# Kernel optimization log

Hardware: AMD Instinct MI355X
Metric: run time of the kernel (lower is better)

Reference implementation:

```python
import jax, jax.numpy as jnp
import numpy as np

B, N, NP, NS = 4, 8192, 2048, 32
CIN, COUT = 128, 256
RADIUS = 0.2
RELU_ALPHA = 0.2
BN_EPS = 1e-5


def setup_inputs() -> dict:
    key = jax.random.key(0)
    k1, k2, k3, k4, k5, k6, k7 = jax.random.split(key, 7)
    xyz = jax.random.uniform(k1, (B, N, 3), dtype=jnp.float32)          # points in unit cube
    feats = jax.random.normal(k2, (B, CIN, N), dtype=jnp.float32)
    conv_w = jax.random.normal(k3, (COUT, CIN), dtype=jnp.float32) * 0.05  # 1x1 conv kernel (bias off: bn=True)
    gamma = jax.random.uniform(k4, (COUT,), minval=0.5, maxval=1.5)
    beta = jax.random.normal(k5, (COUT,)) * 0.1
    rmean = jax.random.normal(k6, (COUT,)) * 0.1                        # BN running mean (eval mode)
    rvar = jax.random.uniform(k7, (COUT,), minval=0.5, maxval=1.5)      # BN running var
    return dict(xyz=xyz, feats=feats, conv_w=conv_w, gamma=gamma,
                beta=beta, rmean=rmean, rvar=rvar)


def _fps(pts):
    """Furthest point sampling. pts: [N,3] -> [NP] int32 indices. Starts at index 0 (CUDA kernel convention)."""
    mind0 = jnp.sum((pts - pts[0]) ** 2, axis=-1)  # [N]

    def step(mind, _):
        i = jnp.argmax(mind)
        mind = jnp.minimum(mind, jnp.sum((pts - pts[i]) ** 2, axis=-1))
        return mind, i.astype(jnp.int32)

    _, idxs = jax.lax.scan(step, mind0, None, length=NP - 1)
    return jnp.concatenate([jnp.zeros((1,), jnp.int32), idxs])


def reference(xyz, feats, conv_w, gamma, beta, rmean, rvar):
    # --- furthest point sampling + gather centroids ---
    fidx = jax.vmap(_fps)(xyz)                                   # [B,NP]
    new_xyz = jnp.take_along_axis(xyz, fidx[:, :, None], axis=1)  # [B,NP,3]

    # --- ball query: first NS point indices (in order) with dist^2 < r^2, pad with first hit ---
    d2 = jnp.sum((new_xyz[:, :, None, :] - xyz[:, None, :, :]) ** 2, axis=-1)  # [B,NP,N]
    mask = d2 < (RADIUS * RADIUS)
    key_ = jnp.where(mask, jnp.arange(N, dtype=jnp.float32), jnp.float32(N))
    neg, _ = jax.lax.top_k(-key_, NS)                            # NS smallest keys
    idx = (-neg).astype(jnp.int32)                               # [B,NP,NS], ascending index order
    first = idx[..., :1]
    fallback = jnp.where(first < N, first, 0)                    # empty ball -> index 0 (kernel default)
    idx = jnp.where(idx < N, idx, fallback)

    # --- grouping + max pool over neighbors ---
    gped = jax.vmap(lambda f, i: f[:, i])(feats, idx)            # [B,CIN,NP,NS]
    pooled = jnp.max(gped, axis=-1)                              # [B,CIN,NP]

    # --- 1x1 conv (no bias) + BatchNorm (eval) + LeakyReLU ---
    out = jnp.einsum('oc,bcn->bon', conv_w, pooled)              # [B,COUT,NP]
    inv = gamma / jnp.sqrt(rvar + BN_EPS)
    out = out * inv[None, :, None] + (beta - rmean * inv)[None, :, None]
    return jax.nn.leaky_relu(out, RELU_ALPHA)
```

## Files before the change

### kernel.cpp

```cpp
#include <hip/hip_runtime.h>
#include <cstdint>
#include <cstddef>

#define BB 4
#define NN 8192
#define NPP 2048
#define NSS 32
#define CINN 128
#define COUTT 256

template<int CTRL>
static __device__ __forceinline__ int dppi(int v){
  return __builtin_amdgcn_update_dpp(0, v, CTRL, 0xF, 0xF, true);
}
template<int CTRL>
static __device__ __forceinline__ float dppf(float v){
  return __int_as_float(__builtin_amdgcn_update_dpp(0, __float_as_int(v), CTRL, 0xF, 0xF, true));
}
static __device__ __forceinline__ float wave_max63(float v){
  v = fmaxf(v, dppf<0xB1>(v));
  v = fmaxf(v, dppf<0x4E>(v));
  v = fmaxf(v, dppf<0x141>(v));
  v = fmaxf(v, dppf<0x140>(v));
  v = fmaxf(v, dppf<0x142>(v));
  v = fmaxf(v, dppf<0x143>(v));
  return v;
}
static __device__ __forceinline__ int wave_mini63(int v){
  v = min(v, dppi<0xB1>(v));
  v = min(v, dppi<0x4E>(v));
  v = min(v, dppi<0x141>(v));
  v = min(v, dppi<0x140>(v));
  v = min(v, dppi<0x142>(v));
  v = min(v, dppi<0x143>(v));
  return v;
}
static __device__ __forceinline__ float red8_maxf(float v){
  v = fmaxf(v, dppf<0xB1>(v));
  v = fmaxf(v, dppf<0x4E>(v));
  v = fmaxf(v, dppf<0x141>(v));
  return v;
}
static __device__ __forceinline__ int red8_mini(int v){
  v = min(v, dppi<0xB1>(v));
  v = min(v, dppi<0x4E>(v));
  v = min(v, dppi<0x141>(v));
  return v;
}

__global__ __launch_bounds__(512)
void k_pre(const float* __restrict__ xyz, const float* __restrict__ feats,
           const float* __restrict__ convw,
           int* __restrict__ fidx, float* __restrict__ featsT, float* __restrict__ wT)
{
  __shared__ float smem[3*NN + 64];
  const int tid = threadIdx.x;
  const int blk = blockIdx.x;

  if (blk < BB) {
    const int b = blk;
    float* xs = smem;
    float* ys = smem + NN;
    float* zs = smem + 2*NN;
    float2* slots = (float2*)(smem + 3*NN);

    for (int n = tid; n < NN; n += 512){
      const float* p = xyz + ((size_t)b*NN + n)*3;
      xs[n] = p[0]; ys[n] = p[1]; zs[n] = p[2];
    }
    __syncthreads();

    float px[16], py[16], pz[16], mind[16];
    const int base = tid*16;
    #pragma unroll
    for (int j=0;j<16;++j){
      px[j]=xs[base+j]; py[j]=ys[base+j]; pz[j]=zs[base+j];
      mind[j]=3.0e38f;
    }
    int cur = 0;
    if (tid == 0) fidx[b*NPP] = 0;
    const int lane = tid & 63;
    const int wid  = tid >> 6;

    for (int s = 1; s < NPP; ++s){
      const float cx = xs[cur], cy = ys[cur], cz = zs[cur];
      float bv = -1.0f; int bj = 0;
      #pragma unroll
      for (int j=0;j<16;++j){
        const float dx = px[j]-cx, dy = py[j]-cy, dz = pz[j]-cz;
        const float d2 = fmaf(dz,dz, fmaf(dy,dy, dx*dx));
        const float m  = fminf(mind[j], d2);
        mind[j] = m;
        const bool g = m > bv;
        bv = g ? m : bv;
        bj = g ? j : bj;
      }
      const int bi = base + bj;

      float wm = wave_max63(bv);
      wm = __int_as_float(__builtin_amdgcn_readlane(__float_as_int(wm), 63));
      int cand = (bv == wm) ? bi : 0x7FFFFFFF;
      int wi = wave_mini63(cand);
      wi = __builtin_amdgcn_readlane(wi, 63);

      const int par = s & 1;
      if (lane == 0) slots[par*8 + wid] = make_float2(wm, __int_as_float(wi));
      __syncthreads();

      const float2 sv = slots[par*8 + (lane & 7)];
      const float v8 = sv.x;
      const int   i8 = __float_as_int(sv.y);
      const float gm = red8_maxf(v8);
      const int   c8 = (v8 == gm) ? i8 : 0x7FFFFFFF;
      cur = red8_mini(c8);

      if (tid == 0) fidx[b*NPP + s] = cur;
    }
  } else if (blk < BB + 2048) {
    const int tb = blk - BB;
    const int b  = tb >> 9;
    const int t  = tb & 511;
    const int r0 = (t & 3) * 32;
    const int c0 = (t >> 2) * 64;
    const float* in = feats + (size_t)b*CINN*NN;
    float* outp = featsT + (size_t)b*NN*CINN;
    float (*tile)[65] = (float(*)[65])smem;
    const int tx = tid & 63, ty = tid >> 6;
    #pragma unroll
    for (int u=0;u<4;++u) tile[ty + 8*u][tx] = in[(size_t)(r0+ty+8*u)*NN + (c0+tx)];
    __syncthreads();
    const int tx2 = tid & 31, ty2 = tid >> 5;
    #pragma unroll
    for (int u=0;u<4;++u) outp[(size_t)(c0+ty2+16*u)*CINN + (r0+tx2)] = tile[tx2][ty2+16*u];
  } else {
    const int t  = blk - BB - 2048;
    const int r0 = (t >> 1) * 32;
    const int c0 = (t & 1) * 64;
    float (*tile)[65] = (float(*)[65])smem;
    const int tx = tid & 63, ty = tid >> 6;
    #pragma unroll
    for (int u=0;u<4;++u) tile[ty+8*u][tx] = convw[(size_t)(r0+ty+8*u)*CINN + (c0+tx)];
    __syncthreads();
    const int tx2 = tid & 31, ty2 = tid >> 5;
    #pragma unroll
    for (int u=0;u<4;++u) wT[(size_t)(c0+ty2+16*u)*COUTT + (r0+tx2)] = tile[tx2][ty2+16*u];
  }
}

__global__ __launch_bounds__(256)
void k_ball(const float* __restrict__ xyz, const int* __restrict__ fidx, int* __restrict__ idxb)
{
  const int lane = threadIdx.x & 63;
  const int gw = blockIdx.x*4 + (threadIdx.x >> 6);
  const int b = gw >> 11;
  const int qi = fidx[gw];
  const float R2F = (float)(0.2 * 0.2);
  const float* q = xyz + ((size_t)b*NN + qi)*3;
  const float qx = q[0], qy = q[1], qz = q[2];
  int* outp = idxb + (size_t)gw*NSS;
  int cnt = 0, first = -1;
  for (int basej = 0; basej < NN; basej += 64){
    const int j = basej + lane;
    const float* P = xyz + ((size_t)b*NN + j)*3;
    const float dx = P[0]-qx, dy = P[1]-qy, dz = P[2]-qz;
    const float d2 = fmaf(dz,dz, fmaf(dy,dy, dx*dx));
    const bool hit = d2 < R2F;
    const unsigned long long m = __ballot(hit);
    if (first < 0 && m != 0ull) first = basej + (int)__builtin_ctzll(m);
    const int slot = cnt + (int)__popcll(m & ((1ull<<lane)-1ull));
    if (hit && slot < NSS) outp[slot] = j;
    cnt += (int)__popcll(m);
    if (cnt >= NSS) break;
  }
  if (cnt < NSS){
    const int f = (first >= 0) ? first : 0;
    if (lane >= cnt && lane < NSS) outp[lane] = f;
  }
}

__global__ __launch_bounds__(256)
void k_pool(const float* __restrict__ featsT, const int* __restrict__ idxb, float* __restrict__ pooledC)
{
  __shared__ int lidx[256];
  const int tid = threadIdx.x;
  const int blk = blockIdx.x;
  lidx[tid] = idxb[(size_t)blk*256 + tid];
  __syncthreads();
  const int hw = tid >> 5, l = tid & 31;
  const int q = blk*8 + hw;
  const int b = q >> 11, p = q & (NPP-1);
  const float4* basep = (const float4*)(featsT + (size_t)b*NN*CINN);
  float4 m = make_float4(-3e38f,-3e38f,-3e38f,-3e38f);
  #pragma unroll 8
  for (int s=0;s<NSS;++s){
    const int i = lidx[hw*32 + s];
    const float4 v = basep[(size_t)i*32 + l];
    m.x = fmaxf(m.x, v.x); m.y = fmaxf(m.y, v.y);
    m.z = fmaxf(m.z, v.z); m.w = fmaxf(m.w, v.w);
  }
  float* oc = pooledC + ((size_t)b*CINN + l*4)*NPP + p;
  oc[0] = m.x; oc[NPP] = m.y; oc[2*(size_t)NPP] = m.z; oc[3*(size_t)NPP] = m.w;
}

__global__ __launch_bounds__(256)
void k_gemm(const float* __restrict__ pooledC, const float* __restrict__ wT,
            const float* __restrict__ gamma, const float* __restrict__ beta,
            const float* __restrict__ rmean, const float* __restrict__ rvar,
            float* __restrict__ out)
{
  const int o = threadIdx.x;
  const int blk = blockIdx.x;
  const int b = blk >> 7;
  const int p0 = (blk & 127) << 4;
  const float* pc = pooledC + (size_t)b*CINN*NPP + p0;
  float acc[16];
  #pragma unroll
  for (int i=0;i<16;++i) acc[i]=0.f;
  #pragma unroll 4
  for (int c=0;c<CINN;++c){
    const float wv = wT[c*COUTT + o];
    const float4* pr = (const float4*)(pc + (size_t)c*NPP);
    #pragma unroll
    for (int qq=0;qq<4;++qq){
      const float4 pv = pr[qq];
      acc[4*qq+0] = fmaf(wv, pv.x, acc[4*qq+0]);
      acc[4*qq+1] = fmaf(wv, pv.y, acc[4*qq+1]);
      acc[4*qq+2] = fmaf(wv, pv.z, acc[4*qq+2]);
      acc[4*qq+3] = fmaf(wv, pv.w, acc[4*qq+3]);
    }
  }
  const float inv = gamma[o] / sqrtf(rvar[o] + 1e-5f);
  const float sh  = beta[o] - rmean[o]*inv;
  float4* op = (float4*)(out + ((size_t)b*COUTT + o)*NPP + p0);
  #pragma unroll
  for (int qq=0;qq<4;++qq){
    float4 y;
    float t0 = fmaf(acc[4*qq+0], inv, sh);
    float t1 = fmaf(acc[4*qq+1], inv, sh);
    float t2 = fmaf(acc[4*qq+2], inv, sh);
    float t3 = fmaf(acc[4*qq+3], inv, sh);
    y.x = t0 >= 0.f ? t0 : 0.2f*t0;
    y.y = t1 >= 0.f ? t1 : 0.2f*t1;
    y.z = t2 >= 0.f ? t2 : 0.2f*t2;
    y.w = t3 >= 0.f ? t3 : 0.2f*t3;
    op[qq] = y;
  }
}

extern "C" void kernel_launch(void* const* d_in, const int* in_sizes, int n_in,
                              void* d_out, int out_size, void* d_ws, size_t ws_size,
                              hipStream_t stream)
{
  (void)in_sizes; (void)n_in; (void)out_size; (void)ws_size;
  const float* xyz   = (const float*)d_in[0];
  const float* feats = (const float*)d_in[1];
  const float* convw = (const float*)d_in[2];
  const float* gamma = (const float*)d_in[3];
  const float* beta  = (const float*)d_in[4];
  const float* rmean = (const float*)d_in[5];
  const float* rvar  = (const float*)d_in[6];
  float* out = (float*)d_out;

  char* ws = (char*)d_ws;
  float* featsT  = (float*)(ws);
  float* pooledC = (float*)(ws + 16777216);
  float* wT      = (float*)(ws + 16777216 + 4194304);
  int*   fidx    = (int*)  (ws + 16777216 + 4194304 + 131072);
  int*   idxb    = (int*)  (ws + 16777216 + 4194304 + 131072 + 32768);

  k_pre <<<dim3(BB + 2048 + 16), dim3(512), 0, stream>>>(xyz, feats, convw, fidx, featsT, wT);
  k_ball<<<dim3(2048),           dim3(256), 0, stream>>>(xyz, fidx, idxb);
  k_pool<<<dim3(1024),           dim3(256), 0, stream>>>(featsT, idxb, pooledC);
  k_gemm<<<dim3(512),            dim3(256), 0, stream>>>(pooledC, wT, gamma, beta, rmean, rvar, out);
}
```

Before: 1.629 ms.

## Broadcast FPS winner coordinates via slots and batch ball-query loads

In the FPS loop, each wave's winner now places its candidate coordinates in the shared slot alongside value and index. The next centroid is then read with readlane instead of a dependent LDS load after the reduction, which shortens the serial critical path of each of the 2047 iterations. FPS indices are buffered in LDS and written out once at the end, and points are stored as float4. Ball query now unrolls four 64-point chunks to issue loads ahead of the ballots, at the cost of sometimes scanning up to 192 extra points past the point where 32 hits are found.

```diff
diff --git a/kernel.cpp b/kernel.cpp
--- a/kernel.cpp
+++ b/kernel.cpp
@@ -53,20 +53,23 @@
            const float* __restrict__ convw,
            int* __restrict__ fidx, float* __restrict__ featsT, float* __restrict__ wT)
 {
-  __shared__ float smem[3*NN + 64];
+  __shared__ union {
+    struct {
+      float4 xyzw[NN];
+      float4 slotA[2][8];
+      float  slotB[2][8];
+      int    sfidx[NPP];
+    } fps;
+    float tile[32][65];
+  } sm;
   const int tid = threadIdx.x;
   const int blk = blockIdx.x;
 
   if (blk < BB) {
     const int b = blk;
-    float* xs = smem;
-    float* ys = smem + NN;
-    float* zs = smem + 2*NN;
-    float2* slots = (float2*)(smem + 3*NN);
-
     for (int n = tid; n < NN; n += 512){
       const float* p = xyz + ((size_t)b*NN + n)*3;
-      xs[n] = p[0]; ys[n] = p[1]; zs[n] = p[2];
+      sm.fps.xyzw[n] = make_float4(p[0], p[1], p[2], 0.f);
     }
     __syncthreads();
 
@@ -74,16 +77,18 @@
     const int base = tid*16;
     #pragma unroll
     for (int j=0;j<16;++j){
-      px[j]=xs[base+j]; py[j]=ys[base+j]; pz[j]=zs[base+j];
+      const float4 p4 = sm.fps.xyzw[base+j];
+      px[j]=p4.x; py[j]=p4.y; pz[j]=p4.z;
       mind[j]=3.0e38f;
     }
-    int cur = 0;
-    if (tid == 0) fidx[b*NPP] = 0;
+    if (tid == 0) sm.fps.sfidx[0] = 0;
     const int lane = tid & 63;
     const int wid  = tid >> 6;
 
+    const float4 c0 = sm.fps.xyzw[0];
+    float cx = c0.x, cy = c0.y, cz = c0.z;
+
     for (int s = 1; s < NPP; ++s){
-      const float cx = xs[cur], cy = ys[cur], cz = zs[cur];
       float bv = -1.0f; int bj = 0;
       #pragma unroll
       for (int j=0;j<16;++j){
@@ -103,19 +108,29 @@
       int wi = wave_mini63(cand);
       wi = __builtin_amdgcn_readlane(wi, 63);
 
+      const float4 cnd = sm.fps.xyzw[wi];
+
       const int par = s & 1;
-      if (lane == 0) slots[par*8 + wid] = make_float2(wm, __int_as_float(wi));
+      if (lane == 0){
+        sm.fps.slotA[par][wid] = make_float4(wm, __int_as_float(wi), cnd.x, cnd.y);
+        sm.fps.slotB[par][wid] = cnd.z;
+      }
       __syncthreads();
 
-      const float2 sv = slots[par*8 + (lane & 7)];
-      const float v8 = sv.x;
-      const int   i8 = __float_as_int(sv.y);
-      const float gm = red8_maxf(v8);
-      const int   c8 = (v8 == gm) ? i8 : 0x7FFFFFFF;
-      cur = red8_mini(c8);
-
-      if (tid == 0) fidx[b*NPP + s] = cur;
-    }
+      const float4 sv  = sm.fps.slotA[par][lane & 7];
+      const float  szv = sm.fps.slotB[par][lane & 7];
+      const float gm = red8_maxf(sv.x);
+      const int   c8 = (sv.x == gm) ? __float_as_int(sv.y) : 0x7FFFFFFF;
+      const int cur  = red8_mini(c8);
+      const int wv   = cur >> 10;
+      cx = __int_as_float(__builtin_amdgcn_readlane(__float_as_int(sv.z), wv));
+      cy = __int_as_float(__builtin_amdgcn_readlane(__float_as_int(sv.w), wv));
+      cz = __int_as_float(__builtin_amdgcn_readlane(__float_as_int(szv),  wv));
+
+      if (tid == 0) sm.fps.sfidx[s] = cur;
+    }
+    __syncthreads();
+    for (int i = tid; i < NPP; i += 512) fidx[b*NPP + i] = sm.fps.sfidx[i];
   } else if (blk < BB + 2048) {
     const int tb = blk - BB;
     const int b  = tb >> 9;
@@ -124,26 +139,24 @@
     const int c0 = (t >> 2) * 64;
     const float* in = feats + (size_t)b*CINN*NN;
     float* outp = featsT + (size_t)b*NN*CINN;
-    float (*tile)[65] = (float(*)[65])smem;
     const int tx = tid & 63, ty = tid >> 6;
     #pragma unroll
-    for (int u=0;u<4;++u) tile[ty + 8*u][tx] = in[(size_t)(r0+ty+8*u)*NN + (c0+tx)];
+    for (int u=0;u<4;++u) sm.tile[ty + 8*u][tx] = in[(size_t)(r0+ty+8*u)*NN + (c0+tx)];
     __syncthreads();
     const int tx2 = tid & 31, ty2 = tid >> 5;
     #pragma unroll
-    for (int u=0;u<4;++u) outp[(size_t)(c0+ty2+16*u)*CINN + (r0+tx2)] = tile[tx2][ty2+16*u];
+    for (int u=0;u<4;++u) outp[(size_t)(c0+ty2+16*u)*CINN + (r0+tx2)] = sm.tile[tx2][ty2+16*u];
   } else {
     const int t  = blk - BB - 2048;
     const int r0 = (t >> 1) * 32;
     const int c0 = (t & 1) * 64;
-    float (*tile)[65] = (float(*)[65])smem;
     const int tx = tid & 63, ty = tid >> 6;
     #pragma unroll
-    for (int u=0;u<4;++u) tile[ty+8*u][tx] = convw[(size_t)(r0+ty+8*u)*CINN + (c0+tx)];
+    for (int u=0;u<4;++u) sm.tile[ty+8*u][tx] = convw[(size_t)(r0+ty+8*u)*CINN + (c0+tx)];
     __syncthreads();
     const int tx2 = tid & 31, ty2 = tid >> 5;
     #pragma unroll
-    for (int u=0;u<4;++u) wT[(size_t)(c0+ty2+16*u)*COUTT + (r0+tx2)] = tile[tx2][ty2+16*u];
+    for (int u=0;u<4;++u) wT[(size_t)(c0+ty2+16*u)*COUTT + (r0+tx2)] = sm.tile[tx2][ty2+16*u];
   }
 }
 
@@ -157,19 +170,26 @@
   const float R2F = (float)(0.2 * 0.2);
   const float* q = xyz + ((size_t)b*NN + qi)*3;
   const float qx = q[0], qy = q[1], qz = q[2];
+  const float* Bp = xyz + (size_t)b*NN*3;
   int* outp = idxb + (size_t)gw*NSS;
   int cnt = 0, first = -1;
-  for (int basej = 0; basej < NN; basej += 64){
-    const int j = basej + lane;
-    const float* P = xyz + ((size_t)b*NN + j)*3;
-    const float dx = P[0]-qx, dy = P[1]-qy, dz = P[2]-qz;
-    const float d2 = fmaf(dz,dz, fmaf(dy,dy, dx*dx));
-    const bool hit = d2 < R2F;
-    const unsigned long long m = __ballot(hit);
-    if (first < 0 && m != 0ull) first = basej + (int)__builtin_ctzll(m);
-    const int slot = cnt + (int)__popcll(m & ((1ull<<lane)-1ull));
-    if (hit && slot < NSS) outp[slot] = j;
-    cnt += (int)__popcll(m);
+  for (int base0 = 0; base0 < NN; base0 += 256){
+    float d2u[4];
+    #pragma unroll
+    for (int u=0;u<4;++u){
+      const float* P = Bp + (size_t)(base0 + u*64 + lane)*3;
+      const float dx = P[0]-qx, dy = P[1]-qy, dz = P[2]-qz;
+      d2u[u] = fmaf(dz,dz, fmaf(dy,dy, dx*dx));
+    }
+    #pragma unroll
+    for (int u=0;u<4;++u){
+      const bool hit = d2u[u] < R2F;
+      const unsigned long long m = __ballot(hit);
+      if (first < 0 && m != 0ull) first = base0 + u*64 + (int)__builtin_ctzll(m);
+      const int slot = cnt + (int)__popcll(m & ((1ull<<lane)-1ull));
+      if (hit && slot < NSS) outp[slot] = base0 + u*64 + lane;
+      cnt += (int)__popcll(m);
+    }
     if (cnt >= NSS) break;
   }
   if (cnt < NSS){
```

New measurement: 1.761 ms. +8.1%, slower.
